# Kernel tuning notes

Hardware: AMD Instinct MI355X
Metric: run time of the kernel (lower is better)

## Reference

```python
import jax, jax.numpy as jnp
import numpy as np

WS = 7      # window_size
NH = 8      # num_heads
ND = 5      # n_degree -> Np = 6


def setup_inputs() -> dict:
    key = jax.random.key(0)
    ks = jax.random.split(key, 9)
    B, Q, C, H, W = 2, 100, 256, 64, 64
    Np = ND + 1
    ws2 = WS * WS
    return {
        "x": jax.random.normal(ks[0], (B, C, H, W), dtype=jnp.float32),
        "polys": jax.random.uniform(ks[1], (B, Q, 2, Np), dtype=jnp.float32),
        "w_qkv": jax.random.normal(ks[2], (3 * C, C), dtype=jnp.float32) * 0.02,
        "b_qkv": jnp.zeros((3 * C,), dtype=jnp.float32),
        "w_proj": jax.random.normal(ks[3], (C, C), dtype=jnp.float32) * 0.02,
        "b_proj": jnp.zeros((C,), dtype=jnp.float32),
        "conv_w": jax.random.normal(ks[4], (1, ws2, 1, 1), dtype=jnp.float32) * 0.1,
        "conv_b": jnp.zeros((1,), dtype=jnp.float32),
        "pos_bias": jax.random.normal(ks[5], (ws2, 1), dtype=jnp.float32),
    }


def reference(x, polys, w_qkv, b_qkv, w_proj, b_proj, conv_w, conv_b, pos_bias):
    B, C, H, W = x.shape
    _, Q, _, Np = polys.shape  # polys: [B,Q,2,n_degree+1]
    ws = WS
    ws2 = ws * ws
    nh = NH
    hd = C // nh
    scale = hd ** -0.5

    # --- polynomial -> sample points (get_points) ---
    alpha = jnp.linspace(0.0, 1.0, Np)
    alphas = jnp.stack([alpha ** i for i in range(Np - 1, -1, -1)], axis=1)  # [Np, Np]
    points = jnp.swapaxes(polys @ alphas.T, -1, -2)  # [B,Q,Np,2]
    points = 2.0 * points - 1.0
    points = points[:, :, None, :, :]  # [B,Q,1,Np,2]

    # --- deformable window grid (faithful to torch, incl. -ws//2 floor-div) ---
    lo = (-ws) // 2   # -4 for ws=7
    hi = ws // 2      #  3
    delta_h = 2.0 * jnp.linspace(lo, hi, ws) / H
    delta_w = 2.0 * jnp.linspace(lo, hi, ws) / W
    mesh_x, mesh_y = jnp.meshgrid(delta_w, delta_h, indexing='xy')  # [ws,ws]
    mesh_x = mesh_x.reshape(-1, 1)  # [ws2,1]
    mesh_y = mesh_y.reshape(-1, 1)
    grid_y = points[..., 0] + mesh_y  # [B,Q,ws2,Np]
    grid_x = points[..., 1] + mesh_x
    grid = jnp.stack((grid_y, grid_x), axis=-1)        # [B,Q,ws2,Np,2]
    grid = grid.reshape(B, Q * Np * ws2, 2)            # same flat order as torch .view

    # --- grid_sample: bilinear, zeros padding, align_corners=True ---
    # grid[...,0] -> x coordinate (width), grid[...,1] -> y (height)
    def sample_one(img, g):  # img [C,H,W], g [P,2] -> [C,P]
        fx = (g[:, 0] + 1.0) * 0.5 * (W - 1)
        fy = (g[:, 1] + 1.0) * 0.5 * (H - 1)
        x0 = jnp.floor(fx)
        y0 = jnp.floor(fy)
        wx1 = fx - x0
        wy1 = fy - y0

        def gather(yy, xx):
            valid = (xx >= 0) & (xx <= W - 1) & (yy >= 0) & (yy <= H - 1)
            xi = jnp.clip(xx, 0, W - 1).astype(jnp.int32)
            yi = jnp.clip(yy, 0, H - 1).astype(jnp.int32)
            return img[:, yi, xi] * valid.astype(img.dtype)  # [C,P]

        v00 = gather(y0, x0)
        v01 = gather(y0, x0 + 1)
        v10 = gather(y0 + 1, x0)
        v11 = gather(y0 + 1, x0 + 1)
        return (v00 * (1 - wy1) * (1 - wx1) + v01 * (1 - wy1) * wx1 +
                v10 * wy1 * (1 - wx1) + v11 * wy1 * wx1)

    sampled = jax.vmap(sample_one)(x, grid)            # [B, C, Q*Np*ws2]
    sampled = sampled.reshape(B, C, Q * Np, ws2)
    sampled = jnp.transpose(sampled, (0, 2, 1, 3))     # [B, Q*Np, C, ws2]
    sp = sampled.reshape(B, Q, Np, C, ws2)
    sp = jnp.transpose(sp, (0, 1, 2, 4, 3)).reshape(B, Q * Np, ws2, C)

    # --- windowed multi-head self-attention over each sampled patch ---
    qkv = sp @ w_qkv.T + b_qkv                          # [B,QN,ws2,3C]
    qkv = qkv.reshape(B, Q * Np, ws2, 3, nh, hd)
    qkv = jnp.transpose(qkv, (3, 0, 4, 1, 2, 5))        # [3,B,nh,QN,ws2,hd]
    q, k, v = qkv[0], qkv[1], qkv[2]
    attn = jnp.einsum('bhnpd,bhnqd->bhnpq', q, k) * scale
    attn = attn + pos_bias.reshape(1, 1, 1, ws2, 1)     # bias per query row (as in torch)
    attn = jax.nn.softmax(attn, axis=-1)
    o = jnp.einsum('bhnpq,bhnqd->bhnpd', attn, v)       # [B,nh,QN,ws2,hd]
    o = jnp.swapaxes(o, 2, 3)                           # [B,nh,ws2,QN,hd]
    o = o.reshape(B, Q * Np, ws2, C)                    # faithful torch .reshape
    o = jnp.swapaxes(o, 1, 2)                           # [B,ws2,QN,C]

    # --- conv1x1 over the ws2 channel axis, then output projection ---
    y = jnp.einsum('bwnc,w->bnc', o, conv_w.reshape(ws2)) + conv_b.reshape(1, 1, 1)
    y = y @ w_proj.T + b_proj                           # [B,QN,C]
    return y.reshape(B, Q, Np, C)
```

## Files before the change

### kernel.cpp

```cpp
#include <hip/hip_runtime.h>

#define B_    2
#define QN    100
#define NP    6
#define WS2   49
#define CC    256
#define NHH   8
#define HDD   32
#define NWIN  600

#define XT_BYTES   (8388608 + 1024)
#define ZABS       2097152
#define WB_BYTES   393216
#define WPT_BYTES  262144

#define SPB_LD 264

#define QK_LD  72
#define VT_LD  72
#define P_LD   72
#define OW_LD  36
#define QK_SHORTS   (WS2 * QK_LD)
#define WREG_SHORTS (QK_SHORTS + 32 * VT_LD)

typedef __attribute__((ext_vector_type(8))) short bf16x8;
typedef __attribute__((ext_vector_type(4))) float f32x4;

__device__ __forceinline__ unsigned short f2bf(float f) {
  union { float f; unsigned int i; } v; v.f = f;
  unsigned int x = v.i;
  x += 0x7fffu + ((x >> 16) & 1u);
  return (unsigned short)(x >> 16);
}
__device__ __forceinline__ float bf2f(unsigned short u) {
  union { unsigned int i; float f; } v; v.i = ((unsigned int)u) << 16; return v.f;
}

__global__ void k0_prep(const float* __restrict__ x, float* __restrict__ xT,
                        const float* __restrict__ w_qkv, unsigned short* __restrict__ wbp,
                        const float* __restrict__ w_proj, float* __restrict__ wpT) {
  __shared__ float tile[32][33];
  const int gb = blockIdx.x;
  if (gb < 2048) {
    int b   = gb >> 10;
    int rem = gb & 1023;
    int hw0 = (rem & 127) * 32;
    int c0  = (rem >> 7) * 32;
    int tx = threadIdx.x & 31, ty = threadIdx.x >> 5;
    const float* src = x + (size_t)b * CC * 4096;
    float* dst = xT + (size_t)b * 4096 * CC;
    #pragma unroll
    for (int i = ty; i < 32; i += 8)
      tile[i][tx] = src[(size_t)(c0 + i) * 4096 + hw0 + tx];
    __syncthreads();
    #pragma unroll
    for (int i = ty; i < 32; i += 8)
      dst[(size_t)(hw0 + i) * CC + c0 + tx] = tile[tx][i];
  } else if (gb < 2144) {
    int g = (gb - 2048) * 256 + threadIdx.x;
    int lane = g & 63;
    int ks = (g >> 6) & 7;
    int nt = g >> 9;
    int n  = nt * 16 + (lane & 15);
    int k0 = ks * 32 + (lane >> 4) * 8;
    const float* src = w_qkv + (size_t)n * CC + k0;
    float4 lo = *(const float4*)(src);
    float4 hi = *(const float4*)(src + 4);
    unsigned short o[8] = { f2bf(lo.x), f2bf(lo.y), f2bf(lo.z), f2bf(lo.w),
                            f2bf(hi.x), f2bf(hi.y), f2bf(hi.z), f2bf(hi.w) };
    *(uint4*)(wbp + (size_t)g * 8) = *(uint4*)o;
  } else if (gb == 2144) {
    xT[ZABS + threadIdx.x] = 0.0f;
  } else {
    int t = gb - 2145;
    int r0 = (t >> 3) * 32;
    int c0 = (t & 7) * 32;
    int tx = threadIdx.x & 31, ty = threadIdx.x >> 5;
    #pragma unroll
    for (int i = ty; i < 32; i += 8)
      tile[i][tx] = w_proj[(size_t)(r0 + i) * CC + c0 + tx];
    __syncthreads();
    #pragma unroll
    for (int i = ty; i < 32; i += 8)
      wpT[(size_t)(c0 + i) * CC + r0 + tx] = tile[tx][i];
  }
}

__device__ __forceinline__ void attn_head(
    const bf16x8 qf[4], const bf16x8 kf[4],
    unsigned short* P, const unsigned short* Vt, float* Ow, unsigned short* ob16,
    int lane, int lm, int lg) {
  const float scale = 0.17677669529663687f;
  f32x4 s[4][4];
  #pragma unroll
  for (int mt = 0; mt < 4; mt++)
    #pragma unroll
    for (int nt = 0; nt < 4; nt++) {
      s[mt][nt] = (f32x4){0.f, 0.f, 0.f, 0.f};
      s[mt][nt] = __builtin_amdgcn_mfma_f32_16x16x32_bf16(qf[mt], kf[nt], s[mt][nt], 0, 0, 0);
    }
  #pragma unroll
  for (int mt = 0; mt < 4; mt++)
    #pragma unroll
    for (int nt = 0; nt < 4; nt++) {
      bool badcol = (nt == 3) && (lm > 0);
      #pragma unroll
      for (int reg = 0; reg < 4; reg++)
        s[mt][nt][reg] = badcol ? -1e30f : s[mt][nt][reg] * scale;
    }
  #pragma unroll
  for (int mt = 0; mt < 4; mt++) {
    #pragma unroll
    for (int reg = 0; reg < 4; reg++) {
      float mx = fmaxf(fmaxf(s[mt][0][reg], s[mt][1][reg]),
                       fmaxf(s[mt][2][reg], s[mt][3][reg]));
      #pragma unroll
      for (int off = 1; off < 16; off <<= 1) mx = fmaxf(mx, __shfl_xor(mx, off));
      float sum = 0.0f;
      #pragma unroll
      for (int nt = 0; nt < 4; nt++) {
        float e = __expf(s[mt][nt][reg] - mx);
        s[mt][nt][reg] = e;
        sum += e;
      }
      #pragma unroll
      for (int off = 1; off < 16; off <<= 1) sum += __shfl_xor(sum, off);
      float inv = 1.0f / sum;
      #pragma unroll
      for (int nt = 0; nt < 4; nt++) s[mt][nt][reg] *= inv;
    }
  }
  #pragma unroll
  for (int mt = 0; mt < 4; mt++)
    #pragma unroll
    for (int nt = 0; nt < 4; nt++)
      #pragma unroll
      for (int reg = 0; reg < 4; reg++) {
        int p = mt * 16 + lg * 4 + reg;
        if (p < WS2) P[p * P_LD + nt * 16 + lm] = f2bf(s[mt][nt][reg]);
      }
  f32x4 o[4][2];
  #pragma unroll
  for (int mt = 0; mt < 4; mt++)
    #pragma unroll
    for (int nt2 = 0; nt2 < 2; nt2++) o[mt][nt2] = (f32x4){0.f, 0.f, 0.f, 0.f};
  #pragma unroll
  for (int ks = 0; ks < 2; ks++) {
    bf16x8 vf[2];
    #pragma unroll
    for (int nt2 = 0; nt2 < 2; nt2++)
      vf[nt2] = *(const bf16x8*)(Vt + (nt2 * 16 + lm) * VT_LD + ks * 32 + lg * 8);
    #pragma unroll
    for (int mt = 0; mt < 4; mt++) {
      bf16x8 af = *(const bf16x8*)(P + (mt * 16 + lm) * P_LD + ks * 32 + lg * 8);
      #pragma unroll
      for (int nt2 = 0; nt2 < 2; nt2++)
        o[mt][nt2] = __builtin_amdgcn_mfma_f32_16x16x32_bf16(af, vf[nt2], o[mt][nt2], 0, 0, 0);
    }
  }
  #pragma unroll
  for (int mt = 0; mt < 4; mt++)
    #pragma unroll
    for (int reg = 0; reg < 4; reg++) {
      int p = mt * 16 + lg * 4 + reg;
      if (p < WS2) {
        #pragma unroll
        for (int nt2 = 0; nt2 < 2; nt2++)
          Ow[p * OW_LD + nt2 * 16 + lm] = o[mt][nt2][reg];
      }
    }
  for (int idx = lane; idx < WS2 * 4; idx += 64) {
    int p = idx >> 2, seg = idx & 3;
    const float* src = Ow + p * OW_LD + seg * 8;
    unsigned short o8[8];
    #pragma unroll
    for (int k = 0; k < 8; k++) o8[k] = f2bf(src[k]);
    *(uint4*)(ob16 + (size_t)idx * 8) = *(uint4*)o8;
  }
}

__launch_bounds__(256, 2)
__global__ void k12_fused(const float* __restrict__ xT,
                          const float* __restrict__ polys,
                          const unsigned short* __restrict__ wbp,
                          const float* __restrict__ b_qkv,
                          unsigned short* __restrict__ o16) {
  __shared__ __align__(16) unsigned short spb[64 * SPB_LD];
  __shared__ __align__(16) unsigned short wreg[4][WREG_SHORTS];
  int*   co_off = (int*)&wreg[0][0];
  float* co_w   = (float*)&wreg[0][0] + 196;
  const int tid = threadIdx.x;
  const int m = (blockIdx.x & 7) * 75 + (blockIdx.x >> 3);
  const int b = blockIdx.y;
  const int lane = tid & 63;
  const int wv = tid >> 6;
  const int lm = lane & 15;
  const int lg = lane >> 4;
  unsigned short* myq = &wreg[wv][0];
  unsigned short* VtW = myq + QK_SHORTS;

  if (tid < WS2) {
    int n = m * WS2 + tid;
    int q = n / (WS2 * NP);
    int p = (n / NP) % WS2;
    int a = n % NP;
    const float* pc = polys + (size_t)(b * QN + q) * 12;
    float al = (float)a * 0.2f;
    float py = pc[0];
    float px = pc[6];
    #pragma unroll
    for (int i = 1; i < 6; i++) { py = py * al + pc[i]; px = px * al + pc[6 + i]; }
    py = 2.0f * py - 1.0f;
    px = 2.0f * px - 1.0f;
    float gy = py + (2.0f * (-4.0f + (float)(p / 7) * (7.0f / 6.0f))) * (1.0f / 64.0f);
    float gx = px + (2.0f * (-4.0f + (float)(p % 7) * (7.0f / 6.0f))) * (1.0f / 64.0f);
    float fx = (gy + 1.0f) * 0.5f * 63.0f;
    float fy = (gx + 1.0f) * 0.5f * 63.0f;
    float x0 = floorf(fx), y0 = floorf(fy);
    float wx = fx - x0, wy = fy - y0;
    float x1 = x0 + 1.0f, y1 = y0 + 1.0f;
    int xi0 = (int)fminf(fmaxf(x0, 0.0f), 63.0f);
    int yi0 = (int)fminf(fmaxf(y0, 0.0f), 63.0f);
    int xi1 = (int)fminf(fmaxf(x1, 0.0f), 63.0f);
    int yi1 = (int)fminf(fmaxf(y1, 0.0f), 63.0f);
    bool vx0 = (x0 >= 0.0f) && (x0 <= 63.0f);
    bool vx1 = (x1 >= 0.0f) && (x1 <= 63.0f);
    bool vy0 = (y0 >= 0.0f) && (y0 <= 63.0f);
    bool vy1 = (y1 >= 0.0f) && (y1 <= 63.0f);
    const int bb = b * 4096;
    co_off[tid * 4 + 0] = (vx0 && vy0) ? (bb + yi0 * 64 + xi0) * CC : ZABS;
    co_off[tid * 4 + 1] = (vx1 && vy0) ? (bb + yi0 * 64 + xi1) * CC : ZABS;
    co_off[tid * 4 + 2] = (vx0 && vy1) ? (bb + yi1 * 64 + xi0) * CC : ZABS;
    co_off[tid * 4 + 3] = (vx1 && vy1) ? (bb + yi1 * 64 + xi1) * CC : ZABS;
    co_w[tid * 4 + 0] = (1.0f - wy) * (1.0f - wx);
    co_w[tid * 4 + 1] = (1.0f - wy) * wx;
    co_w[tid * 4 + 2] = wy * (1.0f - wx);
    co_w[tid * 4 + 3] = wy * wx;
  }
  {
    unsigned int* z = (unsigned int*)(spb + WS2 * SPB_LD);
    for (int i = tid; i < 15 * SPB_LD / 2; i += 256) z[i] = 0u;
  }
  {
    unsigned int* vz = (unsigned int*)VtW;
    #pragma unroll
    for (int i = 0; i < 18; i++) vz[i * 64 + lane] = 0u;
  }
  __syncthreads();

  for (int bi = 0; bi < 6; bi++) {
    const int rbase = bi * 8;
    float vv[8][4];
    #pragma unroll
    for (int k = 0; k < 8; k++) {
      int r = rbase + k;
      int4 off = *(const int4*)&co_off[r * 4];
      vv[k][0] = xT[off.x + tid];
      vv[k][1] = xT[off.y + tid];
      vv[k][2] = xT[off.z + tid];
      vv[k][3] = xT[off.w + tid];
    }
    #pragma unroll
    for (int k = 0; k < 8; k++) {
      int r = rbase + k;
      float4 w = *(const float4*)&co_w[r * 4];
      float s = vv[k][0] * w.x + vv[k][1] * w.y + vv[k][2] * w.z + vv[k][3] * w.w;
      spb[r * SPB_LD + tid] = f2bf(s);
    }
  }
  {
    int4 off = *(const int4*)&co_off[48 * 4];
    float4 w = *(const float4*)&co_w[48 * 4];
    float s = xT[off.x + tid] * w.x + xT[off.y + tid] * w.y
            + xT[off.z + tid] * w.z + xT[off.w + tid] * w.w;
    spb[48 * SPB_LD + tid] = f2bf(s);
  }
  __syncthreads();

  unsigned short* obase = o16 + (size_t)(b * NWIN + m) * 392 * 32;

  for (int hp = 0; hp < 2; hp++) {
    const int h = 2 * wv + hp;
    for (int jc = 0; jc < 3; jc++) {
      const int nt0 = jc * 16 + 2 * h;
      f32x4 acc[4][2];
      #pragma unroll
      for (int j4 = 0; j4 < 2; j4++) {
        float bias = b_qkv[(nt0 + j4) * 16 + lm];
        #pragma unroll
        for (int mt = 0; mt < 4; mt++) acc[mt][j4] = (f32x4){bias, bias, bias, bias};
      }
      bf16x8 bnx[2][2];
      #pragma unroll
      for (int j4 = 0; j4 < 2; j4++) {
        bnx[0][j4] = *(const bf16x8*)(wbp + (size_t)(((nt0 + j4) * 8 + 0) * 64 + lane) * 8);
        bnx[1][j4] = *(const bf16x8*)(wbp + (size_t)(((nt0 + j4) * 8 + 1) * 64 + lane) * 8);
      }
      #pragma unroll
      for (int ks = 0; ks < 8; ks++) {
        bf16x8 bc[2];
        #pragma unroll
        for (int j4 = 0; j4 < 2; j4++) bc[j4] = bnx[ks & 1][j4];
        if (ks < 6) {
          #pragma unroll
          for (int j4 = 0; j4 < 2; j4++)
            bnx[ks & 1][j4] = *(const bf16x8*)(wbp + (size_t)(((nt0 + j4) * 8 + ks + 2) * 64 + lane) * 8);
        }
        bf16x8 af[4];
        #pragma unroll
        for (int mt = 0; mt < 4; mt++)
          af[mt] = *(const bf16x8*)(spb + (mt * 16 + lm) * SPB_LD + ks * 32 + lg * 8);
        #pragma unroll
        for (int j4 = 0; j4 < 2; j4++)
          #pragma unroll
          for (int mt = 0; mt < 4; mt++)
            acc[mt][j4] = __builtin_amdgcn_mfma_f32_16x16x32_bf16(af[mt], bc[j4], acc[mt][j4], 0, 0, 0);
      }
      if (jc < 2) {
        const int cb = jc * 32;
        #pragma unroll
        for (int mt = 0; mt < 4; mt++)
          #pragma unroll
          for (int reg = 0; reg < 4; reg++) {
            int rr = mt * 16 + lg * 4 + reg;
            if (rr < WS2) {
              #pragma unroll
              for (int j4 = 0; j4 < 2; j4++)
                myq[rr * QK_LD + cb + j4 * 16 + lm] = f2bf(acc[mt][j4][reg]);
            }
          }
      } else {
        #pragma unroll
        for (int mt = 0; mt < 4; mt++)
          #pragma unroll
          for (int reg = 0; reg < 4; reg++) {
            int rr = mt * 16 + lg * 4 + reg;
            if (rr < WS2) {
              #pragma unroll
              for (int j4 = 0; j4 < 2; j4++)
                VtW[(j4 * 16 + lm) * VT_LD + rr] = f2bf(acc[mt][j4][reg]);
            }
          }
      }
    }

    bf16x8 qf[4], kf[4];
    #pragma unroll
    for (int t = 0; t < 4; t++) {
      int r = t * 16 + lm; if (r > 48) r = 48;
      const unsigned short* row = myq + r * QK_LD;
      qf[t] = *(const bf16x8*)(row + lg * 8);
      kf[t] = *(const bf16x8*)(row + 32 + lg * 8);
    }
    unsigned short* P = myq;
    float* Ow = (float*)myq;
    attn_head(qf, kf, P, VtW, Ow,
              obase + (size_t)h * WS2 * HDD, lane, lm, lg);
  }
}

__global__ void k3_conv_proj(const unsigned short* __restrict__ o16,
                             const float* __restrict__ conv_w,
                             const float* __restrict__ conv_b,
                             const float* __restrict__ wpT,
                             const float* __restrict__ b_proj,
                             float* __restrict__ out) {
  __shared__ float yv[CC];
  __shared__ float cw[WS2];
  __shared__ int atab[392];
  const int tid = threadIdx.x;
  const int np = blockIdx.x;
  const int b = blockIdx.y;
  if (tid < WS2) cw[tid] = conv_w[tid];
  for (int i = tid; i < 392; i += 256) {
    int Q = np * 392 + i;
    int m = Q % 600;
    int hp = Q / 600;
    atab[i] = ((b * NWIN + m) * 392 + hp) * 32;
  }
  __syncthreads();
  const int cg = tid >> 5, dd = tid & 31;
  float acc = conv_b[0];
  #pragma unroll 1
  for (int pb = 0; pb < 48; pb += 8) {
    float vals[8];
    #pragma unroll
    for (int k = 0; k < 8; k++)
      vals[k] = bf2f(o16[(size_t)atab[(pb + k) * 8 + cg] + dd]);
    #pragma unroll
    for (int k = 0; k < 8; k++) acc += cw[pb + k] * vals[k];
  }
  acc += cw[48] * bf2f(o16[(size_t)atab[48 * 8 + cg] + dd]);
  yv[tid] = acc;
  __syncthreads();
  const float* wp = wpT + tid;
  float a0 = 0.0f, a1 = 0.0f, a2 = 0.0f, a3 = 0.0f;
  #pragma unroll 8
  for (int c = 0; c < CC; c += 4) {
    float4 y4 = *(const float4*)&yv[c];
    a0 += y4.x * wp[(c + 0) * CC];
    a1 += y4.y * wp[(c + 1) * CC];
    a2 += y4.z * wp[(c + 2) * CC];
    a3 += y4.w * wp[(c + 3) * CC];
  }
  out[((size_t)(b * NWIN + np)) * CC + tid] = b_proj[tid] + ((a0 + a1) + (a2 + a3));
}

extern "C" void kernel_launch(void* const* d_in, const int* in_sizes, int n_in,
                              void* d_out, int out_size, void* d_ws, size_t ws_size,
                              hipStream_t stream) {
  const float* x        = (const float*)d_in[0];
  const float* polys    = (const float*)d_in[1];
  const float* w_qkv    = (const float*)d_in[2];
  const float* b_qkv    = (const float*)d_in[3];
  const float* w_proj   = (const float*)d_in[4];
  const float* b_proj   = (const float*)d_in[5];
  const float* conv_w   = (const float*)d_in[6];
  const float* conv_b   = (const float*)d_in[7];
  float* out = (float*)d_out;

  char* ws = (char*)d_ws;
  float* xT = (float*)ws;
  unsigned short* wbp = (unsigned short*)(ws + XT_BYTES);
  float* wpT = (float*)(ws + XT_BYTES + WB_BYTES);
  unsigned short* o16 = (unsigned short*)(ws + XT_BYTES + WB_BYTES + WPT_BYTES);

  hipLaunchKernelGGL(k0_prep, dim3(2209), dim3(256), 0, stream, x, xT, w_qkv, wbp, w_proj, wpT);
  hipLaunchKernelGGL(k12_fused, dim3(NWIN, B_), dim3(256), 0, stream,
                     xT, polys, wbp, b_qkv, o16);
  hipLaunchKernelGGL(k3_conv_proj, dim3(NWIN, B_), dim3(256), 0, stream,
                     o16, conv_w, conv_b, wpT, b_proj, out);
}
```

Before: 169.5 us.

## Fuse conv1x1 reduction into attention kernel via atomic accumulation into y buffer

The attention kernel no longer writes the per-head bf16 output to global memory. Each output element is multiplied by its conv weight and atomically added into a zeroed fp32 y buffer, with the buffer zeroed by extra blocks in the prep kernel. This removes the large o16 round trip and the gather-heavy conv pass. The projection kernel now handles two rows per block so each weight load is reused. The cost is many fp32 global atomics and an accumulation order that is no longer deterministic.

```diff
diff --git a/kernel.cpp b/kernel.cpp
--- a/kernel.cpp
+++ b/kernel.cpp
@@ -19,7 +19,6 @@
 #define QK_LD  72
 #define VT_LD  72
 #define P_LD   72
-#define OW_LD  36
 #define QK_SHORTS   (WS2 * QK_LD)
 #define WREG_SHORTS (QK_SHORTS + 32 * VT_LD)
 
@@ -38,7 +37,8 @@
 
 __global__ void k0_prep(const float* __restrict__ x, float* __restrict__ xT,
                         const float* __restrict__ w_qkv, unsigned short* __restrict__ wbp,
-                        const float* __restrict__ w_proj, float* __restrict__ wpT) {
+                        const float* __restrict__ w_proj, float* __restrict__ wpT,
+                        float* __restrict__ y32) {
   __shared__ float tile[32][33];
   const int gb = blockIdx.x;
   if (gb < 2048) {
@@ -71,7 +71,7 @@
     *(uint4*)(wbp + (size_t)g * 8) = *(uint4*)o;
   } else if (gb == 2144) {
     xT[ZABS + threadIdx.x] = 0.0f;
-  } else {
+  } else if (gb < 2209) {
     int t = gb - 2145;
     int r0 = (t >> 3) * 32;
     int c0 = (t & 7) * 32;
@@ -83,13 +83,16 @@
     #pragma unroll
     for (int i = ty; i < 32; i += 8)
       wpT[(size_t)(c0 + i) * CC + r0 + tx] = tile[tx][i];
+  } else {
+    y32[(size_t)(gb - 2209) * 256 + threadIdx.x] = 0.0f;
   }
 }
 
 __device__ __forceinline__ void attn_head(
     const bf16x8 qf[4], const bf16x8 kf[4],
-    unsigned short* P, const unsigned short* Vt, float* Ow, unsigned short* ob16,
-    int lane, int lm, int lg) {
+    unsigned short* P, const unsigned short* Vt,
+    float* __restrict__ yb, const float* __restrict__ cwl,
+    int m, int h, int lane, int lm, int lg) {
   const float scale = 0.17677669529663687f;
   f32x4 s[4][4];
   #pragma unroll
@@ -164,19 +167,16 @@
     for (int reg = 0; reg < 4; reg++) {
       int p = mt * 16 + lg * 4 + reg;
       if (p < WS2) {
+        int Q = (h * WS2 + p) * 600 + m;
+        int np_ = Q / 392;
+        int r  = Q - np_ * 392;
+        float w = cwl[r >> 3];
+        float* dst = yb + (size_t)np_ * CC + (r & 7) * 32;
         #pragma unroll
         for (int nt2 = 0; nt2 < 2; nt2++)
-          Ow[p * OW_LD + nt2 * 16 + lm] = o[mt][nt2][reg];
-      }
-    }
-  for (int idx = lane; idx < WS2 * 4; idx += 64) {
-    int p = idx >> 2, seg = idx & 3;
-    const float* src = Ow + p * OW_LD + seg * 8;
-    unsigned short o8[8];
-    #pragma unroll
-    for (int k = 0; k < 8; k++) o8[k] = f2bf(src[k]);
-    *(uint4*)(ob16 + (size_t)idx * 8) = *(uint4*)o8;
-  }
+          atomicAdd(dst + nt2 * 16 + lm, w * o[mt][nt2][reg]);
+      }
+    }
 }
 
 __launch_bounds__(256, 2)
@@ -184,9 +184,11 @@
                           const float* __restrict__ polys,
                           const unsigned short* __restrict__ wbp,
                           const float* __restrict__ b_qkv,
-                          unsigned short* __restrict__ o16) {
+                          const float* __restrict__ conv_w,
+                          float* __restrict__ y32) {
   __shared__ __align__(16) unsigned short spb[64 * SPB_LD];
   __shared__ __align__(16) unsigned short wreg[4][WREG_SHORTS];
+  __shared__ float cwl[52];
   int*   co_off = (int*)&wreg[0][0];
   float* co_w   = (float*)&wreg[0][0] + 196;
   const int tid = threadIdx.x;
@@ -199,6 +201,7 @@
   unsigned short* myq = &wreg[wv][0];
   unsigned short* VtW = myq + QK_SHORTS;
 
+  if (tid < WS2) cwl[tid] = conv_w[tid];
   if (tid < WS2) {
     int n = m * WS2 + tid;
     int q = n / (WS2 * NP);
@@ -277,7 +280,7 @@
   }
   __syncthreads();
 
-  unsigned short* obase = o16 + (size_t)(b * NWIN + m) * 392 * 32;
+  float* yb = y32 + (size_t)b * NWIN * CC;
 
   for (int hp = 0; hp < 2; hp++) {
     const int h = 2 * wv + hp;
@@ -353,57 +356,35 @@
       kf[t] = *(const bf16x8*)(row + 32 + lg * 8);
     }
     unsigned short* P = myq;
-    float* Ow = (float*)myq;
-    attn_head(qf, kf, P, VtW, Ow,
-              obase + (size_t)h * WS2 * HDD, lane, lm, lg);
-  }
-}
-
-__global__ void k3_conv_proj(const unsigned short* __restrict__ o16,
-                             const float* __restrict__ conv_w,
-                             const float* __restrict__ conv_b,
-                             const float* __restrict__ wpT,
-                             const float* __restrict__ b_proj,
-                             float* __restrict__ out) {
-  __shared__ float yv[CC];
-  __shared__ float cw[WS2];
-  __shared__ int atab[392];
+    attn_head(qf, kf, P, VtW, yb, cwl, m, h, lane, lm, lg);
+  }
+}
+
+__global__ void k3_proj(const float* __restrict__ y32,
+                        const float* __restrict__ conv_b,
+                        const float* __restrict__ wpT,
+                        const float* __restrict__ b_proj,
+                        float* __restrict__ out) {
+  __shared__ float yv[2][CC];
   const int tid = threadIdx.x;
-  const int np = blockIdx.x;
+  const int np0 = blockIdx.x * 2;
   const int b = blockIdx.y;
-  if (tid < WS2) cw[tid] = conv_w[tid];
-  for (int i = tid; i < 392; i += 256) {
-    int Q = np * 392 + i;
-    int m = Q % 600;
-    int hp = Q / 600;
-    atab[i] = ((b * NWIN + m) * 392 + hp) * 32;
-  }
-  __syncthreads();
-  const int cg = tid >> 5, dd = tid & 31;
-  float acc = conv_b[0];
-  #pragma unroll 1
-  for (int pb = 0; pb < 48; pb += 8) {
-    float vals[8];
-    #pragma unroll
-    for (int k = 0; k < 8; k++)
-      vals[k] = bf2f(o16[(size_t)atab[(pb + k) * 8 + cg] + dd]);
-    #pragma unroll
-    for (int k = 0; k < 8; k++) acc += cw[pb + k] * vals[k];
-  }
-  acc += cw[48] * bf2f(o16[(size_t)atab[48 * 8 + cg] + dd]);
-  yv[tid] = acc;
+  const float cb = conv_b[0];
+  yv[0][tid] = y32[((size_t)b * NWIN + np0) * CC + tid] + cb;
+  yv[1][tid] = y32[((size_t)b * NWIN + np0 + 1) * CC + tid] + cb;
   __syncthreads();
   const float* wp = wpT + tid;
-  float a0 = 0.0f, a1 = 0.0f, a2 = 0.0f, a3 = 0.0f;
+  float a0 = 0.0f, a1 = 0.0f, c0 = 0.0f, c1 = 0.0f;
   #pragma unroll 8
-  for (int c = 0; c < CC; c += 4) {
-    float4 y4 = *(const float4*)&yv[c];
-    a0 += y4.x * wp[(c + 0) * CC];
-    a1 += y4.y * wp[(c + 1) * CC];
-    a2 += y4.z * wp[(c + 2) * CC];
-    a3 += y4.w * wp[(c + 3) * CC];
-  }
-  out[((size_t)(b * NWIN + np)) * CC + tid] = b_proj[tid] + ((a0 + a1) + (a2 + a3));
+  for (int c = 0; c < CC; c += 2) {
+    float w0 = wp[(c + 0) * CC];
+    float w1 = wp[(c + 1) * CC];
+    a0 += yv[0][c] * w0;  a1 += yv[0][c + 1] * w1;
+    c0 += yv[1][c] * w0;  c1 += yv[1][c + 1] * w1;
+  }
+  float bp = b_proj[tid];
+  out[((size_t)(b * NWIN + np0)) * CC + tid]     = bp + (a0 + a1);
+  out[((size_t)(b * NWIN + np0 + 1)) * CC + tid] = bp + (c0 + c1);
 }
 
 extern "C" void kernel_launch(void* const* d_in, const int* in_sizes, int n_in,
@@ -423,11 +404,12 @@
   float* xT = (float*)ws;
   unsigned short* wbp = (unsigned short*)(ws + XT_BYTES);
   float* wpT = (float*)(ws + XT_BYTES + WB_BYTES);
-  unsigned short* o16 = (unsigned short*)(ws + XT_BYTES + WB_BYTES + WPT_BYTES);
-
-  hipLaunchKernelGGL(k0_prep, dim3(2209), dim3(256), 0, stream, x, xT, w_qkv, wbp, w_proj, wpT);
+  float* y32 = (float*)(ws + XT_BYTES + WB_BYTES + WPT_BYTES);
+
+  hipLaunchKernelGGL(k0_prep, dim3(3409), dim3(256), 0, stream,
+                     x, xT, w_qkv, wbp, w_proj, wpT, y32);
   hipLaunchKernelGGL(k12_fused, dim3(NWIN, B_), dim3(256), 0, stream,
-                     xT, polys, wbp, b_qkv, o16);
-  hipLaunchKernelGGL(k3_conv_proj, dim3(NWIN, B_), dim3(256), 0, stream,
-                     o16, conv_w, conv_b, wpT, b_proj, out);
-}
+                     xT, polys, wbp, b_qkv, conv_w, y32);
+  hipLaunchKernelGGL(k3_proj, dim3(NWIN / 2, B_), dim3(256), 0, stream,
+                     y32, conv_b, wpT, b_proj, out);
+}
```

Measured after the change: 190.5 us. +12.4%, slower.
